# Kernel tuning notes

Measured on AMD Instinct MI355X. Metric: run time of the kernel, lower is better.

The kernel has to match this reference:

```python
import jax, jax.numpy as jnp
import numpy as np

B, S, D = 4, 4096, 128

def setup_inputs() -> dict:
    key = jax.random.key(0)
    kx, kq, kk, kv = jax.random.split(key, 4)
    x = jax.random.normal(kx, (B, S, D), dtype=jnp.float32)
    Wq = jax.random.normal(kq, (D, D), dtype=jnp.float32) * (1.0 / np.sqrt(D))
    Wk = jax.random.normal(kk, (D, D), dtype=jnp.float32) * (1.0 / np.sqrt(D))
    Wv = jax.random.normal(kv, (D, D), dtype=jnp.float32) * (1.0 / np.sqrt(D))
    return {"x": x, "Wq": Wq, "Wk": Wk, "Wv": Wv}

def reference(x, Wq, Wk, Wv):
    b, s, d = x.shape
    # nn.Linear(bias=False): y = x @ W.T
    q = jnp.einsum('bsd,ed->bse', x, Wq)
    k = jnp.einsum('bsd,ed->bse', x, Wk)
    v = jnp.einsum('bsd,ed->bse', x, Wv)
    scores = jnp.einsum('bqd,bkd->bqk', q, k) / jnp.sqrt(jnp.float32(d))
    causal = jnp.tril(jnp.ones((s, s), dtype=bool))  # [s,s]
    scores = jnp.where(causal, scores, jnp.float32(-jnp.inf))
    weights = jax.nn.softmax(scores.astype(jnp.float32), axis=-1)
    out = jnp.einsum('bqk,bkd->bqd', weights, v)
    return out  # dropout is identity in eval / p=0
```

## Files before the change

### kernel.cpp

```cpp
#include <hip/hip_runtime.h>
#include <hip/hip_bf16.h>
#include <math.h>

typedef __attribute__((ext_vector_type(8))) short short8;
typedef __attribute__((ext_vector_type(2))) unsigned int uint2v;
typedef __attribute__((ext_vector_type(4))) float f32x4;
typedef __attribute__((ext_vector_type(4))) float float4v;
typedef __attribute__((ext_vector_type(4))) unsigned short ushort4v;

typedef __attribute__((address_space(1))) const unsigned int GAS;
typedef __attribute__((address_space(3))) unsigned int LAS;

#define B_ 4
#define S_ 4096
#define D_ 128

#define CPB 544
#define NSLOT (B_ * CPB)

#define LDS_K 0
#define LDS_V 16384
#define LDS_P 32768
#define LDS_TOTAL 40960

__device__ __forceinline__ unsigned short f2bf(float f) {
    union { float f; unsigned u; } v; v.f = f;
    unsigned r = v.u + 0x7FFFu + ((v.u >> 16) & 1u);
    return (unsigned short)(r >> 16);
}
__device__ __forceinline__ float bf2f(unsigned short h) {
    union { unsigned u; float f; } v; v.u = ((unsigned)h) << 16;
    return v.f;
}
__device__ __forceinline__ unsigned cvt_pk_bf16(float lo, float hi) {
    unsigned r;
    asm("v_cvt_pk_bf16_f32 %0, %1, %2" : "=v"(r) : "v"(lo), "v"(hi));
    return r;
}

__global__ void wconv_kernel(const float* __restrict__ Wq,
                             const float* __restrict__ Wk,
                             const float* __restrict__ Wv,
                             unsigned short* __restrict__ Wb) {
    int i = blockIdx.x * 256 + threadIdx.x;
    if (i >= 3 * 16384) return;
    const float* s = (i < 16384) ? Wq : (i < 32768 ? Wk : Wv);
    Wb[i] = f2bf(s[i & 16383]);
}

__global__ __launch_bounds__(256) void qkv_kernel(const float* __restrict__ X,
                                                  const unsigned short* __restrict__ Wb,
                                                  unsigned short* __restrict__ Qb,
                                                  unsigned short* __restrict__ Kb,
                                                  unsigned short* __restrict__ Vt) {
    const int tid = threadIdx.x;
    const int lane = tid & 63, w = tid >> 6;
    const int l16 = lane & 15, g = lane >> 4;
    const int r0 = blockIdx.x * 64;
    const int grp = blockIdx.y;

    const int row = r0 + w * 16 + l16;
    const float* xr = X + (long)row * 128;
    float4v x0[4], x1[4];
    #pragma unroll
    for (int kb = 0; kb < 4; ++kb) {
        x0[kb] = *reinterpret_cast<const float4v*>(xr + kb * 32 + g * 8);
        x1[kb] = *reinterpret_cast<const float4v*>(xr + kb * 32 + g * 8 + 4);
    }
    short8 a[4];
    #pragma unroll
    for (int kb = 0; kb < 4; ++kb) {
        short8 t;
        t[0] = f2bf(x0[kb][0]); t[1] = f2bf(x0[kb][1]);
        t[2] = f2bf(x0[kb][2]); t[3] = f2bf(x0[kb][3]);
        t[4] = f2bf(x1[kb][0]); t[5] = f2bf(x1[kb][1]);
        t[6] = f2bf(x1[kb][2]); t[7] = f2bf(x1[kb][3]);
        a[kb] = t;
    }

    const float scale = 0.12751744416006513f;
    #pragma unroll
    for (int ct = 0; ct < 8; ++ct) {
        const int e = ct * 16 + l16;
        const int c = grp * 128 + e;
        f32x4 acc = {0.f, 0.f, 0.f, 0.f};
        #pragma unroll
        for (int kb = 0; kb < 4; ++kb) {
            short8 bf = *reinterpret_cast<const short8*>(Wb + (long)c * 128 + kb * 32 + g * 8);
            acc = __builtin_amdgcn_mfma_f32_16x16x32_bf16(a[kb], bf, acc, 0, 0, 0);
        }
        const int row0 = r0 + w * 16 + g * 4;
        if (grp == 0) {
            #pragma unroll
            for (int r = 0; r < 4; ++r) Qb[(long)(row0 + r) * 128 + e] = f2bf(acc[r] * scale);
        } else if (grp == 1) {
            #pragma unroll
            for (int r = 0; r < 4; ++r) Kb[(long)(row0 + r) * 128 + e] = f2bf(acc[r]);
        } else {
            const int bb = row0 >> 12, ss = row0 & 4095;
            ushort4v p;
            p[0] = f2bf(acc[0]); p[1] = f2bf(acc[1]); p[2] = f2bf(acc[2]); p[3] = f2bf(acc[3]);
            *reinterpret_cast<ushort4v*>(&Vt[((long)bb * 128 + e) * 4096 + ss]) = p;
        }
    }
}

__global__ __launch_bounds__(256, 4) void attn_kernel(const unsigned short* __restrict__ Qb,
                                                      const unsigned short* __restrict__ Kb,
                                                      const unsigned short* __restrict__ Vt,
                                                      unsigned short* __restrict__ Opart,
                                                      float* __restrict__ Mpart,
                                                      float* __restrict__ Lpart) {
    __shared__ __align__(16) unsigned char lds[LDS_TOTAL];

    const int tid = threadIdx.x;
    const int lane = tid & 63, w = tid >> 6;
    const int l16 = lane & 15, g = lane >> 4;

    const int bidx = (int)blockIdx.x;
    const int b = bidx / CPB;
    const int rr = CPB - 1 - (bidx - b * CPB);
    int gg = 0;
    while (2 * (gg + 1) * (gg + 2) <= rr) ++gg;
    const int j = rr - 2 * gg * (gg + 1);
    const int qt = 4 * gg + j / (gg + 1);
    const int c = j % (gg + 1);
    const int slot = b * CPB + rr;

    const unsigned short* Qbase = Qb + (long)b * S_ * D_;
    const unsigned char* Kb_b = (const unsigned char*)(Kb + (long)b * S_ * D_);
    const unsigned char* Vb_b = (const unsigned char*)(Vt + (long)b * D_ * S_);

    const int qrow_f = qt * 64 + w * 16 + l16;
    short8 qf[4];
    #pragma unroll
    for (int kb = 0; kb < 4; ++kb)
        qf[kb] = *reinterpret_cast<const short8*>(Qbase + (long)qrow_f * 128 + kb * 32 + g * 8);

    int koff[4], voff[4];
    #pragma unroll
    for (int i = 0; i < 4; ++i) {
        int ch = i * 256 + tid;
        int krow = ch >> 4, kcd = ch & 15;
        koff[i] = krow * 256 + ((kcd * 16) ^ ((krow & 7) << 4));
        int vrow = ch >> 3, vck = ch & 7;
        voff[i] = vrow * 8192 + ((vck * 16) ^ ((vrow & 7) << 4));
    }

    const int swz = (l16 & 7) << 4;
    const unsigned char* kaddr[4];
    const unsigned char* vaddr[2];
    const unsigned char* pread[2];
    unsigned char* pwrite[4];
    unsigned char* Pw = lds + LDS_P + w * 2048;
    #pragma unroll
    for (int i = 0; i < 4; ++i) {
        kaddr[i] = lds + LDS_K + l16 * 256 + ((i * 64 + g * 16) ^ swz);
        pwrite[i] = Pw + l16 * 128 + ((i * 32 + g * 8) ^ swz);
    }
    #pragma unroll
    for (int i = 0; i < 2; ++i) {
        const int xo = (i * 64 + g * 16) ^ swz;
        vaddr[i] = lds + LDS_V + l16 * 128 + xo;
        pread[i] = Pw + l16 * 128 + xo;
    }

    f32x4 o[8];
    #pragma unroll
    for (int dt = 0; dt < 8; ++dt) o[dt] = (f32x4){0.f, 0.f, 0.f, 0.f};
    float m = -INFINITY, lsum = 0.f;
    const int myq = qt * 64 + w * 16 + l16;

    const int kt0 = c * 4;
    const int ktend = min(kt0 + 3, qt);

    for (int kt = kt0; kt <= ktend; ++kt) {
        #pragma unroll
        for (int i = 0; i < 4; ++i) {
            int ch = i * 256 + tid;
            __builtin_amdgcn_global_load_lds((GAS*)(Kb_b + (long)kt * 16384 + koff[i]),
                                             (LAS*)(lds + LDS_K + ch * 16), 16, 0, 0);
            __builtin_amdgcn_global_load_lds((GAS*)(Vb_b + (long)kt * 128 + voff[i]),
                                             (LAS*)(lds + LDS_V + ch * 16), 16, 0, 0);
        }
        __syncthreads();

        f32x4 s[4];
        __builtin_amdgcn_s_setprio(1);
        #pragma unroll
        for (int ct = 0; ct < 4; ++ct) {
            s[ct] = (f32x4){0.f, 0.f, 0.f, 0.f};
            #pragma unroll
            for (int kb = 0; kb < 4; ++kb) {
                short8 kf = *reinterpret_cast<const short8*>(kaddr[kb] + ct * 4096);
                s[ct] = __builtin_amdgcn_mfma_f32_16x16x32_bf16(kf, qf[kb], s[ct], 0, 0, 0);
            }
        }
        __builtin_amdgcn_s_setprio(0);

        if (kt == qt) {
            #pragma unroll
            for (int ct = 0; ct < 4; ++ct) {
                const int kg = kt * 64 + ct * 16 + g * 4;
                #pragma unroll
                for (int r = 0; r < 4; ++r)
                    if (kg + r > myq) s[ct][r] = -1e30f;
            }
        }

        float rmax = s[0][0];
        #pragma unroll
        for (int ct = 0; ct < 4; ++ct) {
            #pragma unroll
            for (int r = 0; r < 4; ++r) rmax = fmaxf(rmax, s[ct][r]);
        }
        rmax = fmaxf(rmax, __shfl_xor(rmax, 16, 64));
        rmax = fmaxf(rmax, __shfl_xor(rmax, 32, 64));
        if (__any(rmax > m + 11.5f)) {
            float mn = fmaxf(m, rmax);
            float al = exp2f(m - mn);
            m = mn;
            lsum *= al;
            #pragma unroll
            for (int dt = 0; dt < 8; ++dt) {
                #pragma unroll
                for (int r = 0; r < 4; ++r) o[dt][r] *= al;
            }
        }
        float rsum = 0.f;
        #pragma unroll
        for (int ct = 0; ct < 4; ++ct) {
            #pragma unroll
            for (int r = 0; r < 4; ++r) {
                float p = exp2f(s[ct][r] - m);
                s[ct][r] = p;
                rsum += p;
            }
        }
        rsum += __shfl_xor(rsum, 16, 64);
        rsum += __shfl_xor(rsum, 32, 64);
        lsum += rsum;

        #pragma unroll
        for (int ct = 0; ct < 4; ++ct) {
            uint2v pb;
            pb[0] = cvt_pk_bf16(s[ct][0], s[ct][1]);
            pb[1] = cvt_pk_bf16(s[ct][2], s[ct][3]);
            *reinterpret_cast<uint2v*>(pwrite[ct]) = pb;
        }

        #pragma unroll
        for (int kvb = 0; kvb < 2; ++kvb) {
            short8 pf = *reinterpret_cast<const short8*>(pread[kvb]);
            __builtin_amdgcn_s_setprio(1);
            #pragma unroll
            for (int dt = 0; dt < 8; ++dt) {
                short8 vf = *reinterpret_cast<const short8*>(vaddr[kvb] + dt * 2048);
                o[dt] = __builtin_amdgcn_mfma_f32_16x16x32_bf16(pf, vf, o[dt], 0, 0, 0);
            }
            __builtin_amdgcn_s_setprio(0);
        }

        if (kt < ktend) __syncthreads();
    }

    unsigned short* Op = Opart + (long)slot * 8192;
    #pragma unroll
    for (int dt = 0; dt < 8; ++dt) {
        #pragma unroll
        for (int r = 0; r < 4; ++r) {
            Op[(w * 16 + g * 4 + r) * 128 + dt * 16 + l16] = f2bf(o[dt][r]);
        }
    }
    if (g == 0) {
        Mpart[(long)slot * 64 + w * 16 + l16] = m;
        Lpart[(long)slot * 64 + w * 16 + l16] = lsum;
    }
}

__global__ __launch_bounds__(256) void combine_kernel(const unsigned short* __restrict__ Opart,
                                                      const float* __restrict__ Mpart,
                                                      const float* __restrict__ Lpart,
                                                      float* __restrict__ out) {
    __shared__ float coeff[16][16];
    __shared__ float invL[16];

    const int qt = blockIdx.x >> 2, qq = blockIdx.x & 3, b = blockIdx.y;
    const int gg = qt >> 2;
    const int nc = gg + 1;
    const int slot0 = b * CPB + 2 * gg * (gg + 1) + (qt - 4 * gg) * nc;
    const int r0 = qq * 16;

    const int tid = threadIdx.x;
    if (tid < 16) {
        float mg = -INFINITY;
        for (int c = 0; c < nc; ++c)
            mg = fmaxf(mg, Mpart[(long)(slot0 + c) * 64 + r0 + tid]);
        float L = 0.f;
        for (int c = 0; c < nc; ++c) {
            float co = exp2f(Mpart[(long)(slot0 + c) * 64 + r0 + tid] - mg);
            coeff[c][tid] = co;
            L += co * Lpart[(long)(slot0 + c) * 64 + r0 + tid];
        }
        invL[tid] = 1.f / L;
    }
    __syncthreads();

    const int e0 = tid * 8;
    const int r = e0 >> 7;
    float acc[8];
    #pragma unroll
    for (int k = 0; k < 8; ++k) acc[k] = 0.f;
    for (int c = 0; c < nc; ++c) {
        short8 v = *reinterpret_cast<const short8*>(Opart + (long)(slot0 + c) * 8192 + r0 * 128 + e0);
        const float co = coeff[c][r];
        #pragma unroll
        for (int k = 0; k < 8; ++k)
            acc[k] += co * bf2f((unsigned short)v[k]);
    }
    const float s = invL[r];
    float4v o0, o1;
    o0[0] = acc[0] * s; o0[1] = acc[1] * s; o0[2] = acc[2] * s; o0[3] = acc[3] * s;
    o1[0] = acc[4] * s; o1[1] = acc[5] * s; o1[2] = acc[6] * s; o1[3] = acc[7] * s;
    float* dst = out + ((long)b * S_ + qt * 64 + r0) * 128 + e0;
    *reinterpret_cast<float4v*>(dst) = o0;
    *reinterpret_cast<float4v*>(dst + 4) = o1;
}

extern "C" void kernel_launch(void* const* d_in, const int* in_sizes, int n_in,
                              void* d_out, int out_size, void* d_ws, size_t ws_size,
                              hipStream_t stream) {
    (void)in_sizes; (void)n_in; (void)out_size; (void)ws_size;
    const float* x  = (const float*)d_in[0];
    const float* Wq = (const float*)d_in[1];
    const float* Wk = (const float*)d_in[2];
    const float* Wv = (const float*)d_in[3];
    float* out = (float*)d_out;

    char* ws = (char*)d_ws;
    const size_t MB4 = (size_t)16384 * 128 * 2;
    unsigned short* Qb = (unsigned short*)(ws);
    unsigned short* Kb = (unsigned short*)(ws + MB4);
    unsigned short* Vt = (unsigned short*)(ws + 2 * MB4);
    unsigned short* Wb = (unsigned short*)(ws + 3 * MB4);
    unsigned short* Opart = (unsigned short*)(ws + 3 * MB4 + (1 << 20));
    float* Mpart = (float*)(ws + 3 * MB4 + (1 << 20) + (size_t)NSLOT * 8192 * 2);
    float* Lpart = Mpart + (size_t)NSLOT * 64;

    wconv_kernel<<<192, 256, 0, stream>>>(Wq, Wk, Wv, Wb);
    qkv_kernel<<<dim3(256, 3), 256, 0, stream>>>(x, Wb, Qb, Kb, Vt);
    attn_kernel<<<NSLOT, 256, 0, stream>>>(Qb, Kb, Vt, Opart, Mpart, Lpart);
    combine_kernel<<<dim3(256, 4), 256, 0, stream>>>(Opart, Mpart, Lpart, out);
}
```

Before: 128.0 us.

## Process 128-row query tiles per attention block to reuse K/V loads

Each attention block now handles two 64-row query groups (a 128-row tile) against the same staged K/V chunk, so every K/V tile loaded into LDS feeds twice as many MFMAs. The chunk-to-slot mapping, partial buffer strides and combine kernel are reworked for the new tiling, and the P scratch area is doubled. In exchange, per-thread register use roughly doubles (two Q fragment sets and two O accumulators), occupancy is lowered to 3 blocks per CU, and the grid is halved, which may hurt load balance.

```diff
diff --git a/kernel.cpp b/kernel.cpp
--- a/kernel.cpp
+++ b/kernel.cpp
@@ -15,13 +15,13 @@
 #define S_ 4096
 #define D_ 128
 
-#define CPB 544
+#define CPB 272
 #define NSLOT (B_ * CPB)
 
 #define LDS_K 0
 #define LDS_V 16384
 #define LDS_P 32768
-#define LDS_TOTAL 40960
+#define LDS_TOTAL 49152
 
 __device__ __forceinline__ unsigned short f2bf(float f) {
     union { float f; unsigned u; } v; v.f = f;
@@ -105,7 +105,7 @@
     }
 }
 
-__global__ __launch_bounds__(256, 4) void attn_kernel(const unsigned short* __restrict__ Qb,
+__global__ __launch_bounds__(256, 3) void attn_kernel(const unsigned short* __restrict__ Qb,
                                                       const unsigned short* __restrict__ Kb,
                                                       const unsigned short* __restrict__ Vt,
                                                       unsigned short* __restrict__ Opart,
@@ -120,22 +120,28 @@
     const int bidx = (int)blockIdx.x;
     const int b = bidx / CPB;
     const int rr = CPB - 1 - (bidx - b * CPB);
-    int gg = 0;
-    while (2 * (gg + 1) * (gg + 2) <= rr) ++gg;
-    const int j = rr - 2 * gg * (gg + 1);
-    const int qt = 4 * gg + j / (gg + 1);
-    const int c = j % (gg + 1);
+    int h = 0;
+    while ((h + 1) * (h + 2) <= rr) ++h;
+    int qt, c;
+    {
+        int rem = rr - h * (h + 1);
+        if (rem < h + 1) { qt = 2 * h; c = rem; }
+        else             { qt = 2 * h + 1; c = rr - (h + 1) * (h + 1); }
+    }
     const int slot = b * CPB + rr;
 
     const unsigned short* Qbase = Qb + (long)b * S_ * D_;
     const unsigned char* Kb_b = (const unsigned char*)(Kb + (long)b * S_ * D_);
     const unsigned char* Vb_b = (const unsigned char*)(Vt + (long)b * D_ * S_);
 
-    const int qrow_f = qt * 64 + w * 16 + l16;
-    short8 qf[4];
-    #pragma unroll
-    for (int kb = 0; kb < 4; ++kb)
-        qf[kb] = *reinterpret_cast<const short8*>(Qbase + (long)qrow_f * 128 + kb * 32 + g * 8);
+    short8 qf[2][4];
+    #pragma unroll
+    for (int cg = 0; cg < 2; ++cg) {
+        const long qrow = qt * 128 + cg * 64 + w * 16 + l16;
+        #pragma unroll
+        for (int kb = 0; kb < 4; ++kb)
+            qf[cg][kb] = *reinterpret_cast<const short8*>(Qbase + qrow * 128 + kb * 32 + g * 8);
+    }
 
     int koff[4], voff[4];
     #pragma unroll
@@ -150,29 +156,35 @@
     const int swz = (l16 & 7) << 4;
     const unsigned char* kaddr[4];
     const unsigned char* vaddr[2];
-    const unsigned char* pread[2];
-    unsigned char* pwrite[4];
-    unsigned char* Pw = lds + LDS_P + w * 2048;
-    #pragma unroll
-    for (int i = 0; i < 4; ++i) {
+    unsigned char* Pw = lds + LDS_P + w * 4096;
+    const unsigned char* pread[2][2];
+    unsigned char* pwrite[2][4];
+    #pragma unroll
+    for (int i = 0; i < 4; ++i)
         kaddr[i] = lds + LDS_K + l16 * 256 + ((i * 64 + g * 16) ^ swz);
-        pwrite[i] = Pw + l16 * 128 + ((i * 32 + g * 8) ^ swz);
-    }
-    #pragma unroll
-    for (int i = 0; i < 2; ++i) {
-        const int xo = (i * 64 + g * 16) ^ swz;
-        vaddr[i] = lds + LDS_V + l16 * 128 + xo;
-        pread[i] = Pw + l16 * 128 + xo;
-    }
-
-    f32x4 o[8];
-    #pragma unroll
-    for (int dt = 0; dt < 8; ++dt) o[dt] = (f32x4){0.f, 0.f, 0.f, 0.f};
-    float m = -INFINITY, lsum = 0.f;
-    const int myq = qt * 64 + w * 16 + l16;
+    #pragma unroll
+    for (int i = 0; i < 2; ++i)
+        vaddr[i] = lds + LDS_V + l16 * 128 + ((i * 64 + g * 16) ^ swz);
+    #pragma unroll
+    for (int cg = 0; cg < 2; ++cg) {
+        #pragma unroll
+        for (int i = 0; i < 2; ++i)
+            pread[cg][i] = Pw + cg * 2048 + l16 * 128 + ((i * 64 + g * 16) ^ swz);
+        #pragma unroll
+        for (int i = 0; i < 4; ++i)
+            pwrite[cg][i] = Pw + cg * 2048 + l16 * 128 + ((i * 32 + g * 8) ^ swz);
+    }
+
+    f32x4 o[2][8];
+    #pragma unroll
+    for (int cg = 0; cg < 2; ++cg)
+        #pragma unroll
+        for (int dt = 0; dt < 8; ++dt) o[cg][dt] = (f32x4){0.f, 0.f, 0.f, 0.f};
+    float m[2] = {-INFINITY, -INFINITY}, lsum[2] = {0.f, 0.f};
+    const int myql = w * 16 + l16;
 
     const int kt0 = c * 4;
-    const int ktend = min(kt0 + 3, qt);
+    const int ktend = min(kt0 + 3, 2 * qt + 1);
 
     for (int kt = kt0; kt <= ktend; ++kt) {
         #pragma unroll
@@ -185,96 +197,109 @@
         }
         __syncthreads();
 
-        f32x4 s[4];
-        __builtin_amdgcn_s_setprio(1);
-        #pragma unroll
-        for (int ct = 0; ct < 4; ++ct) {
-            s[ct] = (f32x4){0.f, 0.f, 0.f, 0.f};
-            #pragma unroll
-            for (int kb = 0; kb < 4; ++kb) {
-                short8 kf = *reinterpret_cast<const short8*>(kaddr[kb] + ct * 4096);
-                s[ct] = __builtin_amdgcn_mfma_f32_16x16x32_bf16(kf, qf[kb], s[ct], 0, 0, 0);
-            }
-        }
-        __builtin_amdgcn_s_setprio(0);
-
-        if (kt == qt) {
+        const int ktl = kt - 2 * qt;
+        #pragma unroll
+        for (int cg = 0; cg < 2; ++cg) {
+            if (cg == 0 && ktl == 1) continue;
+
+            f32x4 s[4];
+            __builtin_amdgcn_s_setprio(1);
             #pragma unroll
             for (int ct = 0; ct < 4; ++ct) {
-                const int kg = kt * 64 + ct * 16 + g * 4;
-                #pragma unroll
-                for (int r = 0; r < 4; ++r)
-                    if (kg + r > myq) s[ct][r] = -1e30f;
-            }
-        }
-
-        float rmax = s[0][0];
-        #pragma unroll
-        for (int ct = 0; ct < 4; ++ct) {
-            #pragma unroll
-            for (int r = 0; r < 4; ++r) rmax = fmaxf(rmax, s[ct][r]);
-        }
-        rmax = fmaxf(rmax, __shfl_xor(rmax, 16, 64));
-        rmax = fmaxf(rmax, __shfl_xor(rmax, 32, 64));
-        if (__any(rmax > m + 11.5f)) {
-            float mn = fmaxf(m, rmax);
-            float al = exp2f(m - mn);
-            m = mn;
-            lsum *= al;
-            #pragma unroll
-            for (int dt = 0; dt < 8; ++dt) {
-                #pragma unroll
-                for (int r = 0; r < 4; ++r) o[dt][r] *= al;
-            }
-        }
-        float rsum = 0.f;
-        #pragma unroll
-        for (int ct = 0; ct < 4; ++ct) {
+                s[ct] = (f32x4){0.f, 0.f, 0.f, 0.f};
+                #pragma unroll
+                for (int kb = 0; kb < 4; ++kb) {
+                    short8 kf = *reinterpret_cast<const short8*>(kaddr[kb] + ct * 4096);
+                    s[ct] = __builtin_amdgcn_mfma_f32_16x16x32_bf16(kf, qf[cg][kb], s[ct], 0, 0, 0);
+                }
+            }
+            __builtin_amdgcn_s_setprio(0);
+
+            if (ktl >= 0) {
+                const int qloc = cg * 64 + myql;
+                #pragma unroll
+                for (int ct = 0; ct < 4; ++ct) {
+                    const int kloc = ktl * 64 + ct * 16 + g * 4;
+                    #pragma unroll
+                    for (int r = 0; r < 4; ++r)
+                        if (kloc + r > qloc) s[ct][r] = -1e30f;
+                }
+            }
+
+            float rmax = s[0][0];
+            #pragma unroll
+            for (int ct = 0; ct < 4; ++ct) {
+                #pragma unroll
+                for (int r = 0; r < 4; ++r) rmax = fmaxf(rmax, s[ct][r]);
+            }
+            rmax = fmaxf(rmax, __shfl_xor(rmax, 16, 64));
+            rmax = fmaxf(rmax, __shfl_xor(rmax, 32, 64));
+            if (__any(rmax > m[cg] + 11.5f)) {
+                float mn = fmaxf(m[cg], rmax);
+                float al = exp2f(m[cg] - mn);
+                m[cg] = mn;
+                lsum[cg] *= al;
+                #pragma unroll
+                for (int dt = 0; dt < 8; ++dt) {
+                    #pragma unroll
+                    for (int r = 0; r < 4; ++r) o[cg][dt][r] *= al;
+                }
+            }
+            float rsum = 0.f;
+            #pragma unroll
+            for (int ct = 0; ct < 4; ++ct) {
+                #pragma unroll
+                for (int r = 0; r < 4; ++r) {
+                    float p = exp2f(s[ct][r] - m[cg]);
+                    s[ct][r] = p;
+                    rsum += p;
+                }
+            }
+            rsum += __shfl_xor(rsum, 16, 64);
+            rsum += __shfl_xor(rsum, 32, 64);
+            lsum[cg] += rsum;
+
+            #pragma unroll
+            for (int ct = 0; ct < 4; ++ct) {
+                uint2v pb;
+                pb[0] = cvt_pk_bf16(s[ct][0], s[ct][1]);
+                pb[1] = cvt_pk_bf16(s[ct][2], s[ct][3]);
+                *reinterpret_cast<uint2v*>(pwrite[cg][ct]) = pb;
+            }
+
+            #pragma unroll
+            for (int kvb = 0; kvb < 2; ++kvb) {
+                short8 pf = *reinterpret_cast<const short8*>(pread[cg][kvb]);
+                __builtin_amdgcn_s_setprio(1);
+                #pragma unroll
+                for (int dt = 0; dt < 8; ++dt) {
+                    short8 vf = *reinterpret_cast<const short8*>(vaddr[kvb] + dt * 2048);
+                    o[cg][dt] = __builtin_amdgcn_mfma_f32_16x16x32_bf16(pf, vf, o[cg][dt], 0, 0, 0);
+                }
+                __builtin_amdgcn_s_setprio(0);
+            }
+        }
+
+        if (kt < ktend) __syncthreads();
+    }
+
+    unsigned short* Op = Opart + (long)slot * 16384;
+    #pragma unroll
+    for (int cg = 0; cg < 2; ++cg) {
+        #pragma unroll
+        for (int dt = 0; dt < 8; ++dt) {
             #pragma unroll
             for (int r = 0; r < 4; ++r) {
-                float p = exp2f(s[ct][r] - m);
-                s[ct][r] = p;
-                rsum += p;
-            }
-        }
-        rsum += __shfl_xor(rsum, 16, 64);
-        rsum += __shfl_xor(rsum, 32, 64);
-        lsum += rsum;
-
-        #pragma unroll
-        for (int ct = 0; ct < 4; ++ct) {
-            uint2v pb;
-            pb[0] = cvt_pk_bf16(s[ct][0], s[ct][1]);
-            pb[1] = cvt_pk_bf16(s[ct][2], s[ct][3]);
-            *reinterpret_cast<uint2v*>(pwrite[ct]) = pb;
-        }
-
-        #pragma unroll
-        for (int kvb = 0; kvb < 2; ++kvb) {
-            short8 pf = *reinterpret_cast<const short8*>(pread[kvb]);
-            __builtin_amdgcn_s_setprio(1);
-            #pragma unroll
-            for (int dt = 0; dt < 8; ++dt) {
-                short8 vf = *reinterpret_cast<const short8*>(vaddr[kvb] + dt * 2048);
-                o[dt] = __builtin_amdgcn_mfma_f32_16x16x32_bf16(pf, vf, o[dt], 0, 0, 0);
-            }
-            __builtin_amdgcn_s_setprio(0);
-        }
-
-        if (kt < ktend) __syncthreads();
-    }
-
-    unsigned short* Op = Opart + (long)slot * 8192;
-    #pragma unroll
-    for (int dt = 0; dt < 8; ++dt) {
-        #pragma unroll
-        for (int r = 0; r < 4; ++r) {
-            Op[(w * 16 + g * 4 + r) * 128 + dt * 16 + l16] = f2bf(o[dt][r]);
+                Op[(cg * 64 + w * 16 + g * 4 + r) * 128 + dt * 16 + l16] = f2bf(o[cg][dt][r]);
+            }
         }
     }
     if (g == 0) {
-        Mpart[(long)slot * 64 + w * 16 + l16] = m;
-        Lpart[(long)slot * 64 + w * 16 + l16] = lsum;
+        #pragma unroll
+        for (int cg = 0; cg < 2; ++cg) {
+            Mpart[(long)slot * 128 + cg * 64 + w * 16 + l16] = m[cg];
+            Lpart[(long)slot * 128 + cg * 64 + w * 16 + l16] = lsum[cg];
+        }
     }
 }
 
@@ -285,22 +310,23 @@
     __shared__ float coeff[16][16];
     __shared__ float invL[16];
 
-    const int qt = blockIdx.x >> 2, qq = blockIdx.x & 3, b = blockIdx.y;
-    const int gg = qt >> 2;
-    const int nc = gg + 1;
-    const int slot0 = b * CPB + 2 * gg * (gg + 1) + (qt - 4 * gg) * nc;
+    const int qt = blockIdx.x >> 3, qq = blockIdx.x & 7, b = blockIdx.y;
+    const int h = qt >> 1;
+    const int nc = h + 1;
+    const int sbase = (qt & 1) ? (h + 1) * (h + 1) : h * (h + 1);
+    const int slot0 = b * CPB + sbase;
     const int r0 = qq * 16;
 
     const int tid = threadIdx.x;
     if (tid < 16) {
         float mg = -INFINITY;
         for (int c = 0; c < nc; ++c)
-            mg = fmaxf(mg, Mpart[(long)(slot0 + c) * 64 + r0 + tid]);
+            mg = fmaxf(mg, Mpart[(long)(slot0 + c) * 128 + r0 + tid]);
         float L = 0.f;
         for (int c = 0; c < nc; ++c) {
-            float co = exp2f(Mpart[(long)(slot0 + c) * 64 + r0 + tid] - mg);
+            float co = exp2f(Mpart[(long)(slot0 + c) * 128 + r0 + tid] - mg);
             coeff[c][tid] = co;
-            L += co * Lpart[(long)(slot0 + c) * 64 + r0 + tid];
+            L += co * Lpart[(long)(slot0 + c) * 128 + r0 + tid];
         }
         invL[tid] = 1.f / L;
     }
@@ -312,7 +338,7 @@
     #pragma unroll
     for (int k = 0; k < 8; ++k) acc[k] = 0.f;
     for (int c = 0; c < nc; ++c) {
-        short8 v = *reinterpret_cast<const short8*>(Opart + (long)(slot0 + c) * 8192 + r0 * 128 + e0);
+        short8 v = *reinterpret_cast<const short8*>(Opart + (long)(slot0 + c) * 16384 + r0 * 128 + e0);
         const float co = coeff[c][r];
         #pragma unroll
         for (int k = 0; k < 8; ++k)
@@ -322,7 +348,7 @@
     float4v o0, o1;
     o0[0] = acc[0] * s; o0[1] = acc[1] * s; o0[2] = acc[2] * s; o0[3] = acc[3] * s;
     o1[0] = acc[4] * s; o1[1] = acc[5] * s; o1[2] = acc[6] * s; o1[3] = acc[7] * s;
-    float* dst = out + ((long)b * S_ + qt * 64 + r0) * 128 + e0;
+    float* dst = out + ((long)b * S_ + qt * 128 + r0) * 128 + e0;
     *reinterpret_cast<float4v*>(dst) = o0;
     *reinterpret_cast<float4v*>(dst + 4) = o1;
 }
@@ -344,8 +370,8 @@
     unsigned short* Vt = (unsigned short*)(ws + 2 * MB4);
     unsigned short* Wb = (unsigned short*)(ws + 3 * MB4);
     unsigned short* Opart = (unsigned short*)(ws + 3 * MB4 + (1 << 20));
-    float* Mpart = (float*)(ws + 3 * MB4 + (1 << 20) + (size_t)NSLOT * 8192 * 2);
-    float* Lpart = Mpart + (size_t)NSLOT * 64;
+    float* Mpart = (float*)(ws + 3 * MB4 + (1 << 20) + (size_t)NSLOT * 16384 * 2);
+    float* Lpart = Mpart + (size_t)NSLOT * 128;
 
     wconv_kernel<<<192, 256, 0, stream>>>(Wq, Wk, Wv, Wb);
     qkv_kernel<<<dim3(256, 3), 256, 0, stream>>>(x, Wb, Qb, Kb, Vt);
```

Result: no change. 129.9 us (+1.4%).
